# Kernel tuning notes

Hardware: AMD Instinct MI355X
Metric: run time of the kernel (lower is better)

Reference implementation:

```python
import jax, jax.numpy as jnp
import numpy as np

B = 4096   # batch
V = 512    # num_variables
H = 64     # hidden_dim


def setup_inputs() -> dict:
    key = jax.random.key(0)
    ks = jax.random.split(key, 6)
    return {
        "X": jax.random.normal(ks[0], (B, V), dtype=jnp.float32),
        "adjacency_logits": jax.random.normal(ks[1], (V, V), dtype=jnp.float32) * 0.1,
        # W1[i] is the first Linear of net i: maps V inputs -> H hidden
        "W1": jax.random.normal(ks[2], (V, V, H), dtype=jnp.float32) * (1.0 / np.sqrt(V)),
        "b1": jax.random.normal(ks[3], (V, H), dtype=jnp.float32) * 0.01,
        # W2[i] is the second Linear of net i: maps H hidden -> 1 output
        "W2": jax.random.normal(ks[4], (V, H), dtype=jnp.float32) * (1.0 / np.sqrt(H)),
        "b2": jax.random.normal(ks[5], (V,), dtype=jnp.float32) * 0.01,
    }


def reference(X, adjacency_logits, W1, b1, W2, b2):
    # Hard adjacency (hard_adjacency=True path): threshold sigmoid, zero diagonal.
    probs = jax.nn.sigmoid(adjacency_logits)
    adj = (probs > 0.5).astype(X.dtype) * (1.0 - jnp.eye(V, dtype=X.dtype))  # [V, V]

    # Original loop: for each i, net_i(X * adj[:, i]).
    # Fold the parent mask into the first-layer weights: W1_eff[i, v, h] = W1[i, v, h] * adj[v, i]
    W1_eff = W1 * adj.T[:, :, None]                      # [V, V, H]
    h = jax.nn.relu(jnp.einsum('bv,ivh->bih', X, W1_eff) + b1[None])  # [B, V, H]
    reconstructed = jnp.einsum('bih,ih->bi', h, W2) + b2[None]        # [B, V]
    return reconstructed, adj
```

## Files before the change

### kernel.cpp

```cpp
#include <hip/hip_runtime.h>
#include <hip/hip_bf16.h>
#include <stdint.h>

#define BB 4096
#define VV 512
#define HH 64

typedef short bf16x8 __attribute__((ext_vector_type(8)));
typedef float floatx4 __attribute__((ext_vector_type(4)));
typedef unsigned short ushort8 __attribute__((ext_vector_type(8)));

typedef const __attribute__((address_space(1))) void g_void;
typedef __attribute__((address_space(3))) void l_void;

__device__ __forceinline__ void gload_lds16(const void* g, void* l) {
    __builtin_amdgcn_global_load_lds((g_void*)g, (l_void*)l, 16, 0, 0);
}

__device__ __forceinline__ unsigned short f2bf_rne(float f) {
    unsigned int u = __float_as_uint(f);
    u += 0x7FFFu + ((u >> 16) & 1u);
    return (unsigned short)(u >> 16);
}

__global__ __launch_bounds__(256) void adj_kernel(const float* __restrict__ logits,
                                                  float* __restrict__ adj_out) {
    int idx = blockIdx.x * 256 + threadIdx.x;
    int v = idx >> 9, u = idx & (VV - 1);
    adj_out[idx] = (logits[idx] > 0.0f && v != u) ? 1.0f : 0.0f;
}

__global__ __launch_bounds__(256) void prep_fused_kernel(
        const float* __restrict__ X, const float* __restrict__ logits,
        const float* __restrict__ W1, float* __restrict__ adj_out,
        unsigned short* __restrict__ Xp, unsigned short* __restrict__ W1t) {
    __shared__ float tile[2][64][65];
    __shared__ float maskv[256];
    int bx = blockIdx.x;
    int t  = threadIdx.x;
    if (bx < 1024) {
        int i  = bx >> 1;
        int v0 = (bx & 1) << 8;
        {
            int v = v0 + t;
            maskv[t] = (logits[(size_t)v * VV + i] > 0.0f && v != i) ? 1.0f : 0.0f;
        }
        const float4* src4 = (const float4*)(W1 + ((size_t)i * VV + v0) * HH);
        unsigned short* dst0 = W1t + (size_t)i * (HH * VV) + v0;

        auto load = [&](int s, int b) {
            #pragma unroll
            for (int jj = 0; jj < 4; ++jj) {
                int c  = jj * 256 + t;
                int vr = c >> 4, h4 = c & 15;
                float4 w = src4[s * 1024 + c];
                tile[b][vr][h4 * 4 + 0] = w.x;
                tile[b][vr][h4 * 4 + 1] = w.y;
                tile[b][vr][h4 * 4 + 2] = w.z;
                tile[b][vr][h4 * 4 + 3] = w.w;
            }
        };
        auto store = [&](int s, int b) {
            #pragma unroll
            for (int j = 0; j < 2; ++j) {
                int c = j * 256 + t;
                int h = c >> 3;
                int vr0 = (c & 7) * 8;
                ushort8 o;
                #pragma unroll
                for (int r = 0; r < 8; ++r)
                    o[r] = f2bf_rne(tile[b][vr0 + r][h] * maskv[s * 64 + vr0 + r]);
                *(ushort8*)&dst0[(size_t)h * VV + s * 64 + vr0] = o;
            }
        };

        load(0, 0);
        __syncthreads();
        #pragma unroll
        for (int s = 0; s < 4; ++s) {
            if (s < 3) load(s + 1, (s + 1) & 1);
            store(s, s & 1);
            __syncthreads();
        }
    } else {
        int idx = (bx - 1024) * 256 + t;
        {
            int v = idx >> 9, u = idx & (VV - 1);
            adj_out[idx] = (logits[idx] > 0.0f && v != u) ? 1.0f : 0.0f;
        }
        {
            int row = idx >> 6;
            int k0  = (idx & 63) << 3;
            const float4* s4 = (const float4*)(X + (size_t)row * VV + k0);
            float4 a = s4[0], b = s4[1];
            ushort8 o;
            o[0] = f2bf_rne(a.x); o[1] = f2bf_rne(a.y);
            o[2] = f2bf_rne(a.z); o[3] = f2bf_rne(a.w);
            o[4] = f2bf_rne(b.x); o[5] = f2bf_rne(b.y);
            o[6] = f2bf_rne(b.z); o[7] = f2bf_rne(b.w);
            int rb = row >> 6, mt = (row >> 4) & 3, lnr = row & 15;
            int ks = k0 >> 5, quad = (k0 >> 3) & 3;
            size_t chunk = (((size_t)(rb * 16 + ks) * 4 + mt) << 6) + quad * 16 + lnr;
            *(ushort8*)(Xp + chunk * 8) = o;
        }
    }
}

__global__ __launch_bounds__(256, 2) void dag_gemm_kernel(
        const unsigned short* __restrict__ Xp,
        const unsigned short* __restrict__ W1t,
        const float* __restrict__ b1,
        const float* __restrict__ W2,
        const float* __restrict__ b2,
        float* __restrict__ out)
{
    __shared__ __align__(16) unsigned short Ws[2][16384];
    __shared__ float Po[2][256];

    const int t    = threadIdx.x;
    const int wave = t >> 6;
    const int lane = t & 63;
    const int ln   = lane & 15;
    const int quad = lane >> 4;

    const int bx   = blockIdx.x;
    const int i0   = (bx >> 4) << 1;
    const int row0 = (bx & 15) << 8;

    auto ldb = [&](int ii, int pos, int nt) -> bf16x8 {
        return *(const bf16x8*)&Ws[ii][(nt * 16 + ln) * 256 + ((pos ^ (ln & 7)) * 8)];
    };

    const unsigned short* abase =
        Xp + (size_t)((row0 >> 6) + wave) * (64 * VV) + lane * 8;

    bf16x8 af[2][4];
    #pragma unroll
    for (int mt = 0; mt < 4; ++mt)
        af[0][mt] = *(const bf16x8*)(abase + mt * 512);

    const unsigned short* wb0 = W1t + (size_t)i0 * (HH * VV);
    const unsigned short* wb1 = W1t + (size_t)(i0 + 1) * (HH * VV);
    auto stage = [&](int kb) {
        #pragma unroll
        for (int j = 0; j < 8; ++j) {
            int c = j * 256 + t;
            int h = c >> 5, s2 = c & 31;
            size_t off = (size_t)h * VV + (size_t)(kb + (s2 ^ (h & 7))) * 8;
            gload_lds16(wb0 + off, (char*)&Ws[0][0] + c * 16);
            gload_lds16(wb1 + off, (char*)&Ws[1][0] + c * 16);
        }
    };
    stage(0);
    __syncthreads();

    floatx4 acc[2][4][4];
    #pragma unroll
    for (int ii = 0; ii < 2; ++ii)
        #pragma unroll
        for (int a = 0; a < 4; ++a)
            #pragma unroll
            for (int b = 0; b < 4; ++b)
                acc[ii][a][b] = (floatx4){0.f, 0.f, 0.f, 0.f};

    bf16x8 bq[2][2][4];
    #pragma unroll
    for (int ii = 0; ii < 2; ++ii)
        #pragma unroll
        for (int nt = 0; nt < 4; ++nt)
            bq[0][ii][nt] = ldb(ii, quad, nt);

    #pragma unroll
    for (int kk = 0; kk < 8; ++kk) {
        #pragma unroll
        for (int mt = 0; mt < 4; ++mt)
            af[(kk + 1) & 1][mt] =
                *(const bf16x8*)(abase + ((kk + 1) * 4 + mt) * 512);
        if (kk < 7) {
            #pragma unroll
            for (int ii = 0; ii < 2; ++ii)
                #pragma unroll
                for (int nt = 0; nt < 4; ++nt)
                    bq[(kk + 1) & 1][ii][nt] = ldb(ii, (kk + 1) * 4 + quad, nt);
        }
        #pragma unroll
        for (int ii = 0; ii < 2; ++ii)
            #pragma unroll
            for (int mt = 0; mt < 4; ++mt)
                #pragma unroll
                for (int nt = 0; nt < 4; ++nt)
                    acc[ii][mt][nt] = __builtin_amdgcn_mfma_f32_16x16x32_bf16(
                        af[kk & 1][mt], bq[kk & 1][ii][nt], acc[ii][mt][nt], 0, 0, 0);
    }

    __syncthreads();

    stage(32);
    __syncthreads();

    #pragma unroll
    for (int ii = 0; ii < 2; ++ii)
        #pragma unroll
        for (int nt = 0; nt < 4; ++nt)
            bq[0][ii][nt] = ldb(ii, quad, nt);

    #pragma unroll
    for (int kk = 8; kk < 16; ++kk) {
        if (kk < 15) {
            #pragma unroll
            for (int mt = 0; mt < 4; ++mt)
                af[(kk + 1) & 1][mt] =
                    *(const bf16x8*)(abase + ((kk + 1) * 4 + mt) * 512);
            #pragma unroll
            for (int ii = 0; ii < 2; ++ii)
                #pragma unroll
                for (int nt = 0; nt < 4; ++nt)
                    bq[(kk + 1) & 1][ii][nt] = ldb(ii, ((kk + 1) - 8) * 4 + quad, nt);
        }
        #pragma unroll
        for (int ii = 0; ii < 2; ++ii)
            #pragma unroll
            for (int mt = 0; mt < 4; ++mt)
                #pragma unroll
                for (int nt = 0; nt < 4; ++nt)
                    acc[ii][mt][nt] = __builtin_amdgcn_mfma_f32_16x16x32_bf16(
                        af[kk & 1][mt], bq[kk & 1][ii][nt], acc[ii][mt][nt], 0, 0, 0);
    }

    float b1v[2][4], w2v[2][4], b2i[2];
    #pragma unroll
    for (int ii = 0; ii < 2; ++ii) {
        #pragma unroll
        for (int nt = 0; nt < 4; ++nt) {
            b1v[ii][nt] = b1[(i0 + ii) * HH + nt * 16 + ln];
            w2v[ii][nt] = W2[(i0 + ii) * HH + nt * 16 + ln];
        }
        b2i[ii] = b2[i0 + ii];
    }
    #pragma unroll
    for (int ii = 0; ii < 2; ++ii) {
        #pragma unroll
        for (int mt = 0; mt < 4; ++mt) {
            #pragma unroll
            for (int r = 0; r < 4; ++r) {
                float p = 0.f;
                #pragma unroll
                for (int nt = 0; nt < 4; ++nt) {
                    float hv = acc[ii][mt][nt][r] + b1v[ii][nt];
                    hv = hv > 0.f ? hv : 0.f;
                    p += hv * w2v[ii][nt];
                }
                p += __shfl_xor(p, 8);
                p += __shfl_xor(p, 4);
                p += __shfl_xor(p, 2);
                p += __shfl_xor(p, 1);
                if (ln == 0)
                    Po[ii][wave * 64 + mt * 16 + quad * 4 + r] = p + b2i[ii];
            }
        }
    }
    const int row = row0 + wave * 64 + lane;
    out[(size_t)row * VV + i0]     = Po[0][wave * 64 + lane];
    out[(size_t)row * VV + i0 + 1] = Po[1][wave * 64 + lane];
}

__global__ __launch_bounds__(256) void fallback_kernel(
        const float* __restrict__ X, const float* __restrict__ logits,
        const float* __restrict__ W1, const float* __restrict__ b1,
        const float* __restrict__ W2, const float* __restrict__ b2,
        float* __restrict__ out) {
    __shared__ float Wc[128][64];
    int i   = blockIdx.x & (VV - 1);
    int row = (blockIdx.x >> 9) * 256 + threadIdx.x;
    float acc[64];
    #pragma unroll
    for (int h = 0; h < 64; ++h) acc[h] = 0.f;
    for (int v0 = 0; v0 < VV; v0 += 128) {
        __syncthreads();
        for (int j = 0; j < 32; ++j) {
            int idx = j * 256 + threadIdx.x;
            int vr = idx >> 6, h = idx & 63;
            int v = v0 + vr;
            float m = (logits[(size_t)v * VV + i] > 0.f && v != i) ? 1.f : 0.f;
            Wc[vr][h] = W1[((size_t)i * VV + v) * HH + h] * m;
        }
        __syncthreads();
        for (int vr = 0; vr < 128; ++vr) {
            float xv = X[(size_t)row * VV + v0 + vr];
            #pragma unroll
            for (int h = 0; h < 64; ++h) acc[h] += xv * Wc[vr][h];
        }
    }
    float p = b2[i];
    #pragma unroll
    for (int h = 0; h < 64; ++h) {
        float hv = acc[h] + b1[i * HH + h];
        p += (hv > 0.f ? hv : 0.f) * W2[i * HH + h];
    }
    out[(size_t)row * VV + i] = p;
}

extern "C" void kernel_launch(void* const* d_in, const int* in_sizes, int n_in,
                              void* d_out, int out_size, void* d_ws, size_t ws_size,
                              hipStream_t stream) {
    const float* X      = (const float*)d_in[0];
    const float* logits = (const float*)d_in[1];
    const float* W1     = (const float*)d_in[2];
    const float* b1     = (const float*)d_in[3];
    const float* W2     = (const float*)d_in[4];
    const float* b2     = (const float*)d_in[5];

    float* out     = (float*)d_out;
    float* adj_out = out + (size_t)BB * VV;

    const size_t xp_bytes  = (size_t)BB * VV * 2;
    const size_t w1t_bytes = (size_t)VV * HH * VV * 2;
    const size_t need = xp_bytes + w1t_bytes;

    if (ws_size >= need) {
        unsigned short* Xp  = (unsigned short*)d_ws;
        unsigned short* W1t = (unsigned short*)((char*)d_ws + xp_bytes);
        hipLaunchKernelGGL(prep_fused_kernel, dim3(2048), dim3(256), 0, stream,
                           X, logits, W1, adj_out, Xp, W1t);
        hipLaunchKernelGGL(dag_gemm_kernel, dim3(4096), dim3(256), 0, stream,
                           Xp, W1t, b1, W2, b2, out);
    } else {
        hipLaunchKernelGGL(adj_kernel, dim3((VV * VV) / 256), dim3(256), 0, stream,
                           logits, adj_out);
        hipLaunchKernelGGL(fallback_kernel, dim3(VV * (BB / 256)), dim3(256), 0, stream,
                           X, logits, W1, b1, W2, b2, out);
    }
}
```

Before: 239.2 us.

## Keep per-net weights resident in LDS and loop blocks over all batch rows

Each block now loads the full bf16 first-layer weights for its two nets into shared memory once, then iterates over all batch rows in 64-row chunks per wave. This replaces the previous grid where each of 4096 blocks re-staged the same weights in two K halves, aiming to cut repeated global weight traffic and staging barriers. The exchange is a much smaller grid (256 blocks of 512 threads) with large LDS use, which limits occupancy and latency hiding.

```diff
diff --git a/kernel.cpp b/kernel.cpp
--- a/kernel.cpp
+++ b/kernel.cpp
@@ -106,7 +106,7 @@
     }
 }
 
-__global__ __launch_bounds__(256, 2) void dag_gemm_kernel(
+__global__ __launch_bounds__(512, 2) void dag_gemm_kernel(
         const unsigned short* __restrict__ Xp,
         const unsigned short* __restrict__ W1t,
         const float* __restrict__ b1,
@@ -114,8 +114,8 @@
         const float* __restrict__ b2,
         float* __restrict__ out)
 {
-    __shared__ __align__(16) unsigned short Ws[2][16384];
-    __shared__ float Po[2][256];
+    __shared__ __align__(16) unsigned short Ws[2][32768];
+    __shared__ float Po[2][512];
 
     const int t    = threadIdx.x;
     const int wave = t >> 6;
@@ -123,109 +123,31 @@
     const int ln   = lane & 15;
     const int quad = lane >> 4;
 
-    const int bx   = blockIdx.x;
-    const int i0   = (bx >> 4) << 1;
-    const int row0 = (bx & 15) << 8;
+    const int i0 = blockIdx.x << 1;
 
     auto ldb = [&](int ii, int pos, int nt) -> bf16x8 {
-        return *(const bf16x8*)&Ws[ii][(nt * 16 + ln) * 256 + ((pos ^ (ln & 7)) * 8)];
+        return *(const bf16x8*)&Ws[ii][(nt * 16 + ln) * 512 + ((pos ^ (ln & 7)) * 8)];
     };
 
-    const unsigned short* abase =
-        Xp + (size_t)((row0 >> 6) + wave) * (64 * VV) + lane * 8;
-
     bf16x8 af[2][4];
+    const unsigned short* ab0 =
+        Xp + (size_t)(wave * 8) * (64 * VV) + lane * 8;
     #pragma unroll
     for (int mt = 0; mt < 4; ++mt)
-        af[0][mt] = *(const bf16x8*)(abase + mt * 512);
-
-    const unsigned short* wb0 = W1t + (size_t)i0 * (HH * VV);
-    const unsigned short* wb1 = W1t + (size_t)(i0 + 1) * (HH * VV);
-    auto stage = [&](int kb) {
-        #pragma unroll
-        for (int j = 0; j < 8; ++j) {
-            int c = j * 256 + t;
-            int h = c >> 5, s2 = c & 31;
-            size_t off = (size_t)h * VV + (size_t)(kb + (s2 ^ (h & 7))) * 8;
-            gload_lds16(wb0 + off, (char*)&Ws[0][0] + c * 16);
-            gload_lds16(wb1 + off, (char*)&Ws[1][0] + c * 16);
-        }
-    };
-    stage(0);
+        af[0][mt] = *(const bf16x8*)(ab0 + mt * 512);
+
+    {
+        const unsigned short* wb = W1t + (size_t)i0 * (HH * VV);
+        #pragma unroll
+        for (int j = 0; j < 16; ++j) {
+            int c  = j * 512 + t;
+            int ii = c >> 12, h = (c >> 6) & 63, s2 = c & 63;
+            gload_lds16(wb + (size_t)ii * (HH * VV) + (size_t)h * VV
+                           + (size_t)(s2 ^ (h & 7)) * 8,
+                        (char*)Ws + c * 16);
+        }
+    }
     __syncthreads();
-
-    floatx4 acc[2][4][4];
-    #pragma unroll
-    for (int ii = 0; ii < 2; ++ii)
-        #pragma unroll
-        for (int a = 0; a < 4; ++a)
-            #pragma unroll
-            for (int b = 0; b < 4; ++b)
-                acc[ii][a][b] = (floatx4){0.f, 0.f, 0.f, 0.f};
-
-    bf16x8 bq[2][2][4];
-    #pragma unroll
-    for (int ii = 0; ii < 2; ++ii)
-        #pragma unroll
-        for (int nt = 0; nt < 4; ++nt)
-            bq[0][ii][nt] = ldb(ii, quad, nt);
-
-    #pragma unroll
-    for (int kk = 0; kk < 8; ++kk) {
-        #pragma unroll
-        for (int mt = 0; mt < 4; ++mt)
-            af[(kk + 1) & 1][mt] =
-                *(const bf16x8*)(abase + ((kk + 1) * 4 + mt) * 512);
-        if (kk < 7) {
-            #pragma unroll
-            for (int ii = 0; ii < 2; ++ii)
-                #pragma unroll
-                for (int nt = 0; nt < 4; ++nt)
-                    bq[(kk + 1) & 1][ii][nt] = ldb(ii, (kk + 1) * 4 + quad, nt);
-        }
-        #pragma unroll
-        for (int ii = 0; ii < 2; ++ii)
-            #pragma unroll
-            for (int mt = 0; mt < 4; ++mt)
-                #pragma unroll
-                for (int nt = 0; nt < 4; ++nt)
-                    acc[ii][mt][nt] = __builtin_amdgcn_mfma_f32_16x16x32_bf16(
-                        af[kk & 1][mt], bq[kk & 1][ii][nt], acc[ii][mt][nt], 0, 0, 0);
-    }
-
-    __syncthreads();
-
-    stage(32);
-    __syncthreads();
-
-    #pragma unroll
-    for (int ii = 0; ii < 2; ++ii)
-        #pragma unroll
-        for (int nt = 0; nt < 4; ++nt)
-            bq[0][ii][nt] = ldb(ii, quad, nt);
-
-    #pragma unroll
-    for (int kk = 8; kk < 16; ++kk) {
-        if (kk < 15) {
-            #pragma unroll
-            for (int mt = 0; mt < 4; ++mt)
-                af[(kk + 1) & 1][mt] =
-                    *(const bf16x8*)(abase + ((kk + 1) * 4 + mt) * 512);
-            #pragma unroll
-            for (int ii = 0; ii < 2; ++ii)
-                #pragma unroll
-                for (int nt = 0; nt < 4; ++nt)
-                    bq[(kk + 1) & 1][ii][nt] = ldb(ii, ((kk + 1) - 8) * 4 + quad, nt);
-        }
-        #pragma unroll
-        for (int ii = 0; ii < 2; ++ii)
-            #pragma unroll
-            for (int mt = 0; mt < 4; ++mt)
-                #pragma unroll
-                for (int nt = 0; nt < 4; ++nt)
-                    acc[ii][mt][nt] = __builtin_amdgcn_mfma_f32_16x16x32_bf16(
-                        af[kk & 1][mt], bq[kk & 1][ii][nt], acc[ii][mt][nt], 0, 0, 0);
-    }
 
     float b1v[2][4], w2v[2][4], b2i[2];
     #pragma unroll
@@ -237,31 +159,90 @@
         }
         b2i[ii] = b2[i0 + ii];
     }
-    #pragma unroll
-    for (int ii = 0; ii < 2; ++ii) {
-        #pragma unroll
-        for (int mt = 0; mt < 4; ++mt) {
-            #pragma unroll
-            for (int r = 0; r < 4; ++r) {
-                float p = 0.f;
-                #pragma unroll
-                for (int nt = 0; nt < 4; ++nt) {
-                    float hv = acc[ii][mt][nt][r] + b1v[ii][nt];
-                    hv = hv > 0.f ? hv : 0.f;
-                    p += hv * w2v[ii][nt];
+
+    bf16x8 bq[2][2][4];
+    #pragma unroll
+    for (int ii = 0; ii < 2; ++ii)
+        #pragma unroll
+        for (int nt = 0; nt < 4; ++nt)
+            bq[0][ii][nt] = ldb(ii, quad, nt);
+
+    #pragma unroll 1
+    for (int c = 0; c < 8; ++c) {
+        const unsigned short* ab =
+            Xp + (size_t)(wave * 8 + c) * (64 * VV) + lane * 8;
+        const unsigned short* abn = ab + 64 * VV;
+
+        floatx4 acc[2][4][4];
+        #pragma unroll
+        for (int ii = 0; ii < 2; ++ii)
+            #pragma unroll
+            for (int a = 0; a < 4; ++a)
+                #pragma unroll
+                for (int b = 0; b < 4; ++b)
+                    acc[ii][a][b] = (floatx4){0.f, 0.f, 0.f, 0.f};
+
+        #pragma unroll
+        for (int kk = 0; kk < 16; ++kk) {
+            if (kk < 15) {
+                #pragma unroll
+                for (int mt = 0; mt < 4; ++mt)
+                    af[(kk + 1) & 1][mt] =
+                        *(const bf16x8*)(ab + ((kk + 1) * 4 + mt) * 512);
+            } else if (c < 7) {
+                #pragma unroll
+                for (int mt = 0; mt < 4; ++mt)
+                    af[0][mt] = *(const bf16x8*)(abn + mt * 512);
+            }
+            if (kk < 15) {
+                #pragma unroll
+                for (int ii = 0; ii < 2; ++ii)
+                    #pragma unroll
+                    for (int nt = 0; nt < 4; ++nt)
+                        bq[(kk + 1) & 1][ii][nt] = ldb(ii, (kk + 1) * 4 + quad, nt);
+            } else if (c < 7) {
+                #pragma unroll
+                for (int ii = 0; ii < 2; ++ii)
+                    #pragma unroll
+                    for (int nt = 0; nt < 4; ++nt)
+                        bq[0][ii][nt] = ldb(ii, quad, nt);
+            }
+            #pragma unroll
+            for (int ii = 0; ii < 2; ++ii)
+                #pragma unroll
+                for (int mt = 0; mt < 4; ++mt)
+                    #pragma unroll
+                    for (int nt = 0; nt < 4; ++nt)
+                        acc[ii][mt][nt] = __builtin_amdgcn_mfma_f32_16x16x32_bf16(
+                            af[kk & 1][mt], bq[kk & 1][ii][nt], acc[ii][mt][nt], 0, 0, 0);
+        }
+
+        #pragma unroll
+        for (int ii = 0; ii < 2; ++ii) {
+            #pragma unroll
+            for (int mt = 0; mt < 4; ++mt) {
+                #pragma unroll
+                for (int r = 0; r < 4; ++r) {
+                    float p = 0.f;
+                    #pragma unroll
+                    for (int nt = 0; nt < 4; ++nt) {
+                        float hv = acc[ii][mt][nt][r] + b1v[ii][nt];
+                        hv = hv > 0.f ? hv : 0.f;
+                        p += hv * w2v[ii][nt];
+                    }
+                    p += __shfl_xor(p, 8);
+                    p += __shfl_xor(p, 4);
+                    p += __shfl_xor(p, 2);
+                    p += __shfl_xor(p, 1);
+                    if (ln == 0)
+                        Po[ii][wave * 64 + mt * 16 + quad * 4 + r] = p + b2i[ii];
                 }
-                p += __shfl_xor(p, 8);
-                p += __shfl_xor(p, 4);
-                p += __shfl_xor(p, 2);
-                p += __shfl_xor(p, 1);
-                if (ln == 0)
-                    Po[ii][wave * 64 + mt * 16 + quad * 4 + r] = p + b2i[ii];
-            }
-        }
-    }
-    const int row = row0 + wave * 64 + lane;
-    out[(size_t)row * VV + i0]     = Po[0][wave * 64 + lane];
-    out[(size_t)row * VV + i0 + 1] = Po[1][wave * 64 + lane];
+            }
+        }
+        const int row = (wave * 8 + c) * 64 + lane;
+        out[(size_t)row * VV + i0]     = Po[0][wave * 64 + lane];
+        out[(size_t)row * VV + i0 + 1] = Po[1][wave * 64 + lane];
+    }
 }
 
 __global__ __launch_bounds__(256) void fallback_kernel(
@@ -322,7 +303,7 @@
         unsigned short* W1t = (unsigned short*)((char*)d_ws + xp_bytes);
         hipLaunchKernelGGL(prep_fused_kernel, dim3(2048), dim3(256), 0, stream,
                            X, logits, W1, adj_out, Xp, W1t);
-        hipLaunchKernelGGL(dag_gemm_kernel, dim3(4096), dim3(256), 0, stream,
+        hipLaunchKernelGGL(dag_gemm_kernel, dim3(256), dim3(512), 0, stream,
                            Xp, W1t, b1, W2, b2, out);
     } else {
         hipLaunchKernelGGL(adj_kernel, dim3((VV * VV) / 256), dim3(256), 0, stream,
```

After: 643.3 us. 2.69x slower.
